# Kernel optimization log

Measured on AMD Instinct MI355X. Metric: run time of the kernel, lower is better.

Reference implementation:

```python
import jax, jax.numpy as jnp
import numpy as np

FEATURE_DIM = 16
NUM_HEADS = 16
HEAD_DIM = 64
R2 = float(np.sqrt(2.0))
RD = float(np.sqrt(FEATURE_DIM))        # sqrt(d) = 4
RRD = float(np.sqrt(RD))                # d^(1/4) = 2
RMS_EPS = 1e-5


def taylor_exp(x):
    # x: [b, h, l, d] -> [b, h, l, 1 + d + d*d]
    x2 = (x[..., :, None] * x[..., None, :]).reshape(*x.shape[:-1], FEATURE_DIM * FEATURE_DIM) / R2
    ones = jnp.ones_like(x[..., :1])
    return jnp.concatenate([ones, x / RRD, x2 / RD], axis=-1)


def setup_inputs() -> dict:
    key = jax.random.key(0)
    ks = jax.random.split(key, 5)
    b, l, d_model = 4, 2048, 1024
    inp = {
        'hidden_states': jax.random.normal(ks[0], (b, l, d_model), dtype=jnp.float32),
        'Wq': jax.random.normal(ks[1], (FEATURE_DIM * NUM_HEADS, d_model), dtype=jnp.float32) * 0.02,
        'Wk': jax.random.normal(ks[2], (FEATURE_DIM * NUM_HEADS, d_model), dtype=jnp.float32) * 0.02,
        'Wv': jax.random.normal(ks[3], (NUM_HEADS * HEAD_DIM, d_model), dtype=jnp.float32) * 0.02,
        'Wo': jax.random.normal(ks[4], (d_model, NUM_HEADS * HEAD_DIM), dtype=jnp.float32) * 0.02,
        'g_weight': jnp.ones((HEAD_DIM,), dtype=jnp.float32),
    }
    return inp


def reference(hidden_states, Wq, Wk, Wv, Wo, g_weight):
    b, l, _ = hidden_states.shape
    # projections (Linear, no bias): x @ W.T
    q = (hidden_states @ Wq.T).reshape(b, l, NUM_HEADS, FEATURE_DIM).transpose(0, 2, 1, 3)
    k = (hidden_states @ Wk.T).reshape(b, l, NUM_HEADS, FEATURE_DIM).transpose(0, 2, 1, 3)
    v = (hidden_states @ Wv.T).reshape(b, l, NUM_HEADS, HEAD_DIM).transpose(0, 2, 1, 3)

    qf = taylor_exp(q)  # [b, h, l, 273]
    kf = taylor_exp(k)  # [b, h, l, 273]

    A_qk = jnp.einsum('bhnd,bhmd->bhnm', qf, kf)
    A_qk = jnp.tril(A_qk)
    y = jnp.einsum('bhnm,bhme->bhne', A_qk, v)  # [b, h, l, head_dim]

    kv_state = jnp.einsum('bhnd,bhnf->bhfd', kf, v)[:, :, None]  # [b, h, 1, head_dim, 273]

    # RMSNorm over head_dim
    rms = jax.lax.rsqrt(jnp.mean(y * y, axis=-1, keepdims=True) + RMS_EPS)
    y = y * rms * g_weight

    y = y.transpose(0, 2, 1, 3).reshape(b, l, NUM_HEADS * HEAD_DIM)
    out = y @ Wo.T
    return out, kv_state
```

## Files before the change

kernel.cpp:

```cpp
#include <hip/hip_runtime.h>


typedef unsigned short u16;
typedef unsigned int u32;
typedef __attribute__((ext_vector_type(4))) float f32x4;
typedef __attribute__((ext_vector_type(16))) float f32x16;
typedef __attribute__((ext_vector_type(8))) short s16x8;

struct MaskT { static constexpr bool value = true;  };
struct MaskF { static constexpr bool value = false; };

__device__ __forceinline__ float bf2f(u16 u) {
    union { unsigned int i; float f; } x; x.i = ((unsigned int)u) << 16; return x.f;
}
__device__ __forceinline__ u16 f2bf(float f) {
    union { float f; unsigned int u; } x; x.f = f;
    unsigned int r = x.u + 0x7FFFu + ((x.u >> 16) & 1u);
    return (u16)(r >> 16);
}

typedef const __attribute__((address_space(1))) u32* gas1_t;
typedef __attribute__((address_space(3))) u32* las3_t;
__device__ __forceinline__ void gld16(const u16* g, u16* l) {
    __builtin_amdgcn_global_load_lds((gas1_t)(const void*)g, (las3_t)(void*)l, 16, 0, 0);
}

__global__ void detect_kernel(const unsigned int* __restrict__ H, int* __restrict__ flag)
{
    const int lane = threadIdx.x;
    int cnt = 0;
#pragma unroll
    for (int i = 0; i < 16; ++i) {
        const unsigned int wrd = H[lane * 16 + i];
        const int e = (int)((wrd >> 7) & 0xFFu);
        if (e >= 85 && e <= 170) ++cnt;
    }
    cnt += __shfl_xor(cnt, 1);  cnt += __shfl_xor(cnt, 2);
    cnt += __shfl_xor(cnt, 4);  cnt += __shfl_xor(cnt, 8);
    cnt += __shfl_xor(cnt, 16); cnt += __shfl_xor(cnt, 32);
    if (lane == 0) *flag = (cnt < 700) ? 1 : 0;
}

__global__ __launch_bounds__(256)
void cvt_all_kernel(const void* __restrict__ H,  const void* __restrict__ Wq,
                    const void* __restrict__ Wk, const void* __restrict__ Wv,
                    const void* __restrict__ Wo, const void* __restrict__ gw,
                    u16* __restrict__ Hb,  u16* __restrict__ Wqb,
                    u16* __restrict__ Wkb, u16* __restrict__ Wvb,
                    u16* __restrict__ Wob, u16* __restrict__ gwb,
                    const int* __restrict__ flag)
{
    const int f32in = *flag;
    const int NQ = 11010112 / 4;
    for (int qi = blockIdx.x * 256 + threadIdx.x; qi < NQ; qi += gridDim.x * 256) {
        const int i = qi * 4;
        const void* src; u16* dst; int off;
        if      (i <  8388608) { src = H;  dst = Hb;  off = i; }
        else if (i <  8650752) { src = Wq; dst = Wqb; off = i - 8388608; }
        else if (i <  8912896) { src = Wk; dst = Wkb; off = i - 8650752; }
        else if (i <  9961472) { src = Wv; dst = Wvb; off = i - 8912896; }
        else if (i < 11010048) { src = Wo; dst = Wob; off = i - 9961472; }
        else                   { src = gw; dst = gwb; off = i - 11010048; }
        ushort4 o;
        if (f32in) {
            const float4 v = *((const float4*)src + (off >> 2));
            o.x = f2bf(v.x); o.y = f2bf(v.y); o.z = f2bf(v.z); o.w = f2bf(v.w);
        } else {
            o = *((const ushort4*)src + (off >> 2));
        }
        *(ushort4*)(dst + off) = o;
    }
}

template<int MODE>
__global__ __launch_bounds__(256)
void gemm_nt(const u16* __restrict__ A,
             const u16* __restrict__ Bq, const u16* __restrict__ Bk,
             const u16* __restrict__ Bv,
             u16* __restrict__ Oq, u16* __restrict__ Ok,
             u16* __restrict__ Ovt, float* __restrict__ Of)
{
    __shared__ __attribute__((aligned(16))) u16 As[4096];
    __shared__ __attribute__((aligned(16))) u16 Bs[4096];
    const int t = threadIdx.x;
    const int lane = t & 63, w = t >> 6;
    const int c = lane & 15, qd = lane >> 4;
    const int wm = (w >> 1) * 64, wn = (w & 1) * 64;
    const int rm = blockIdx.y * 128;
    const int cb = blockIdx.x * 128;

    const u16* Bsrc; int wrow0;
    if (MODE == 0) {
        if (cb < 256)      { Bsrc = Bq; wrow0 = cb; }
        else if (cb < 512) { Bsrc = Bk; wrow0 = cb - 256; }
        else               { Bsrc = Bv; wrow0 = cb - 512; }
    } else { Bsrc = Bq; wrow0 = cb; }

    f32x4 acc[4][4];
#pragma unroll
    for (int i = 0; i < 4; ++i)
#pragma unroll
        for (int j = 0; j < 4; ++j) acc[i][j] = (f32x4){0.f, 0.f, 0.f, 0.f};

    const u16* Ag = A    + (size_t)(rm    + (t >> 2)) * 1024 + (t & 3) * 8;
    const u16* Bg = Bsrc + (size_t)(wrow0 + (t >> 2)) * 1024 + (t & 3) * 8;
    u16* AsW = As + w * 512;
    u16* BsW = Bs + w * 512;

    for (int kt = 0; kt < 32; ++kt) {
        const int k0 = kt * 32;
        __syncthreads();
        gld16(Ag + k0,         AsW);
        gld16(Ag + 65536 + k0, AsW + 2048);
        gld16(Bg + k0,         BsW);
        gld16(Bg + 65536 + k0, BsW + 2048);
        __syncthreads();
        s16x8 af[4], bfr[4];
#pragma unroll
        for (int mt = 0; mt < 4; ++mt) af[mt]  = *(const s16x8*)&As[(wm + mt * 16 + c) * 32 + qd * 8];
#pragma unroll
        for (int nt = 0; nt < 4; ++nt) bfr[nt] = *(const s16x8*)&Bs[(wn + nt * 16 + c) * 32 + qd * 8];
#pragma unroll
        for (int mt = 0; mt < 4; ++mt)
#pragma unroll
            for (int nt = 0; nt < 4; ++nt)
                acc[mt][nt] = __builtin_amdgcn_mfma_f32_16x16x32_bf16(af[mt], bfr[nt], acc[mt][nt], 0, 0, 0);
    }

#pragma unroll
    for (int mt = 0; mt < 4; ++mt) {
#pragma unroll
        for (int nt = 0; nt < 4; ++nt) {
            const int gc = cb + wn + nt * 16 + c;
            const int row0 = rm + wm + mt * 16 + qd * 4;
            if (MODE == 1) {
#pragma unroll
                for (int r = 0; r < 4; ++r)
                    Of[(size_t)(row0 + r) * 1024 + gc] = acc[mt][nt][r];
            } else if (gc < 512) {
#pragma unroll
                for (int r = 0; r < 4; ++r) {
                    const int row = row0 + r;
                    const int b_ = row >> 11, l_ = row & 2047;
                    const int cc = gc & 255;
                    const int h = cc >> 4, idx = cc & 15;
                    u16* dst = (gc < 256) ? Oq : Ok;
                    dst[(size_t)((b_ * 16 + h) * 2048 + l_) * 16 + idx] = f2bf(acc[mt][nt][r]);
                }
            } else {
                const int cc = gc - 512;
                const int h = cc >> 6, idx = cc & 63;
                const int b_ = row0 >> 11, l0 = row0 & 2047;
                ushort4 pk;
                pk.x = f2bf(acc[mt][nt][0]);
                pk.y = f2bf(acc[mt][nt][1]);
                pk.z = f2bf(acc[mt][nt][2]);
                pk.w = f2bf(acc[mt][nt][3]);
                *(ushort4*)(Ovt + ((size_t)((b_ * 16 + h) * 64 + idx)) * 2048 + l0) = pk;
            }
        }
    }
}

__global__ __launch_bounds__(512, 2)
void attn_kernel(const u16* __restrict__ Qg, const u16* __restrict__ Kg,
                 const u16* __restrict__ Vt, const u16* __restrict__ gwb,
                 u16* __restrict__ Yn)
{
    __shared__ __attribute__((aligned(16))) u16 Vs[2][8192];
    const int t = threadIdx.x, lane = t & 63, w = t >> 6;
    const int la = lane & 31, h = lane >> 5;
    const int pid = blockIdx.y * 4 + blockIdx.x;
    const int lid = (pid & 7) * 32 + (pid >> 3);
    const int bh = lid >> 2;
    const int jj = lid & 3;
    const int b_ = bh >> 4, hh = bh & 15;
    const u16* Qh = Qg + (size_t)bh * (2048 * 16);
    const u16* Kh = Kg + (size_t)bh * (2048 * 16);
    const u16* Vh = Vt + (size_t)bh * (64 * 2048);
    const float gl0 = bf2f(gwb[la]);
    const float gl1 = bf2f(gwb[32 + la]);
    const f32x16 z16 = {0.f,0.f,0.f,0.f,0.f,0.f,0.f,0.f,
                        0.f,0.f,0.f,0.f,0.f,0.f,0.f,0.f};
    const int vbase0 = (la << 8) | (h << 4);
    const int vsw = (la & 7) << 4;

    auto stageV = [&](int n0s, int bufsel) {
#pragma unroll
        for (int i = 0; i < 2; ++i) {
            const int slot = i * 512 + t;
            const int fl = slot >> 4;
            const int seg = (slot & 15) ^ (fl & 7);
            gld16(Vh + (size_t)fl * 2048 + n0s + seg * 8,
                  (u16*)Vs[bufsel] + (size_t)(i * 512 + (w << 6)) * 8);
        }
    };

    for (int pass = 0; pass < 2; ++pass) {
        const int qb = pass ? jj : (7 - jj);
        const int q0 = qb * 256 + w * 32;
        const int kf = 2 * qb + (w >> 2);
        const int wp = w & 3;
        const int nck = 2 * qb + 2;

        const s16x8 bq = *(const s16x8*)(Qh + (size_t)(q0 + la) * 16 + h * 8);
        f32x16 yt0 = z16, yt1 = z16;
        s16x8 ka[4];
        const char* vsc = (const char*)Vs[0];

        auto loadK = [&](s16x8* kk, int kcL) {
#pragma unroll
            for (int kt = 0; kt < 4; ++kt)
                kk[kt] = *(const s16x8*)(Kh + (size_t)(kcL * 128 + kt * 32 + la) * 16 + h * 8);
        };

        auto tile = [&](int kt, auto MASKED) {
            constexpr bool masked = decltype(MASKED)::value;
            f32x16 sv = __builtin_amdgcn_mfma_f32_32x32x16_bf16(ka[kt], bq, z16, 0, 0, 0);
            float p[16];
#pragma unroll
            for (int r = 0; r < 16; ++r) {
                const float s = sv[r];
                float pv = fmaf(s, fmaf(s, 0.03125f, 0.25f), 1.0f);
                if (masked) {
                    const int keyloc = (r & 3) + 8 * (r >> 2) + 4 * h;
                    if (keyloc > la) pv = 0.f;
                }
                p[r] = pv;
            }
#pragma unroll
            for (int ks = 0; ks < 2; ++ks) {
                u32 X0, X1, Y0, Y1;
                asm("v_cvt_pk_bf16_f32 %0, %1, %2" : "=v"(X0) : "v"(p[8*ks+0]), "v"(p[8*ks+1]));
                asm("v_cvt_pk_bf16_f32 %0, %1, %2" : "=v"(X1) : "v"(p[8*ks+2]), "v"(p[8*ks+3]));
                asm("v_cvt_pk_bf16_f32 %0, %1, %2" : "=v"(Y0) : "v"(p[8*ks+4]), "v"(p[8*ks+5]));
                asm("v_cvt_pk_bf16_f32 %0, %1, %2" : "=v"(Y1) : "v"(p[8*ks+6]), "v"(p[8*ks+7]));
                asm("v_permlane32_swap_b32 %0, %1" : "+v"(X0), "+v"(Y0));
                asm("v_permlane32_swap_b32 %0, %1" : "+v"(X1), "+v"(Y1));
                union { uint4 u; s16x8 v; } afu;
                afu.u = (uint4){X0, X1, Y0, Y1};
                const int offb = (kt << 6) | (ks << 5);
                const s16x8 vb0 = *(const s16x8*)(vsc + (((vbase0 + offb)) ^ vsw));
                const s16x8 vb1 = *(const s16x8*)(vsc + (((vbase0 + 8192 + offb)) ^ vsw));
                yt0 = __builtin_amdgcn_mfma_f32_32x32x16_bf16(afu.v, vb0, yt0, 0, 0, 0);
                yt1 = __builtin_amdgcn_mfma_f32_32x32x16_bf16(afu.v, vb1, yt1, 0, 0, 0);
            }
        };

        stageV(0, 0);
        loadK(ka, 0);
        __syncthreads();

        for (int kc = 0; kc < nck; ++kc) {
            const int cur = kc & 1;
            vsc = (const char*)Vs[cur];
            if (kc + 1 < nck) stageV((kc + 1) * 128, cur ^ 1);
            s16x8 kn[4] = {ka[0], ka[1], ka[2], ka[3]};
            if (kc < kf) loadK(kn, kc + 1);

            if (kc < kf) {
                tile(0, MaskF{}); tile(1, MaskF{});
                tile(2, MaskF{}); tile(3, MaskF{});
            } else if (kc == kf) {
                if (wp == 0)      { tile(0, MaskT{}); }
                else if (wp == 1) { tile(0, MaskF{}); tile(1, MaskT{}); }
                else if (wp == 2) { tile(0, MaskF{}); tile(1, MaskF{}); tile(2, MaskT{}); }
                else              { tile(0, MaskF{}); tile(1, MaskF{}); tile(2, MaskF{}); tile(3, MaskT{}); }
            }
            __syncthreads();
#pragma unroll
            for (int kt = 0; kt < 4; ++kt) ka[kt] = kn[kt];
        }

#pragma unroll
        for (int r = 0; r < 16; ++r) {
            float ss = yt0[r] * yt0[r] + yt1[r] * yt1[r];
            ss += __shfl_xor(ss, 1);  ss += __shfl_xor(ss, 2);
            ss += __shfl_xor(ss, 4);  ss += __shfl_xor(ss, 8);
            ss += __shfl_xor(ss, 16);
            const float rmsv = rsqrtf(ss * (1.0f / 64.0f) + 1e-5f);
            const int row = q0 + (r & 3) + 8 * (r >> 2) + 4 * h;
            u16* dst = Yn + ((size_t)(b_ * 2048 + row)) * 1024 + hh * 64;
            dst[la]      = f2bf(yt0[r] * rmsv * gl0);
            dst[32 + la] = f2bf(yt1[r] * rmsv * gl1);
        }
    }
}

__global__ __launch_bounds__(256)
void kv_mfma_kernel(const u16* __restrict__ Kg, const u16* __restrict__ Vt,
                    float* __restrict__ kvpart)
{
    __shared__ __attribute__((aligned(16))) float kS[64][20];
    __shared__ __attribute__((aligned(16))) float kT[64][20];
    __shared__ __attribute__((aligned(16))) u16 KFs[288][72];
    __shared__ __attribute__((aligned(16))) u16 Vs[64][72];
    const int t = threadIdx.x, lane = t & 63, w = t >> 6;
    const int c = lane & 15, qd = lane >> 4;
    const int ns = blockIdx.x, bh = blockIdx.y;
    const u16* Kh  = Kg + (size_t)bh * 2048 * 16;
    const u16* Vth = Vt + (size_t)bh * 64 * 2048;

    int i2a, j2a, i2b = 18, j2b = 18;
    {
        const int dd = t;
        if (dd == 0)      { i2a = 16; j2a = 17; }
        else if (dd < 17) { i2a = dd - 1; j2a = 16; }
        else              { i2a = (dd - 17) >> 4; j2a = (dd - 17) & 15; }
        if (t < 32) {
            const int d2 = 256 + t;
            if (d2 < 273) { i2b = (d2 - 17) >> 4; j2b = (d2 - 17) & 15; }
        }
    }

    f32x4 acc[4][5];
#pragma unroll
    for (int mt = 0; mt < 4; ++mt)
#pragma unroll
        for (int j = 0; j < 5; ++j) acc[mt][j] = (f32x4){0.f, 0.f, 0.f, 0.f};

    for (int ch = 0; ch < 8; ++ch) {
        const int n0 = ns * 512 + ch * 64;
        __syncthreads();
        if (t < 128) {
            const int row = t >> 1, half = t & 1;
            uint4 kv = *(const uint4*)(Kh + (size_t)(n0 + row) * 16 + half * 8);
            const u16* ke = (const u16*)&kv;
#pragma unroll
            for (int e = 0; e < 8; ++e) {
                const float f = bf2f(ke[e]);
                kS[row][half * 8 + e] = f;
                kT[row][half * 8 + e] = f * 0.17677669529663687f;
            }
        } else if (t < 192) {
            const int row = t - 128;
            kS[row][16] = 1.f;  kS[row][17] = 1.f;  kS[row][18] = 0.f;
            kT[row][16] = 0.5f; kT[row][17] = 1.f;  kT[row][18] = 0.f;
        }
#pragma unroll
        for (int i = 0; i < 2; ++i) {
            const int lin = i * 256 + t;
            const int f = lin >> 3, seg = lin & 7;
            *(uint4*)&Vs[f][seg * 8] =
                *(const uint4*)(Vth + (size_t)f * 2048 + n0 + seg * 8);
        }
        __syncthreads();
        {
            unsigned int* dst = (unsigned int*)&KFs[t][0];
#pragma unroll 8
            for (int i = 0; i < 32; ++i) {
                const float v0 = kS[2 * i][i2a]     * kT[2 * i][j2a];
                const float v1 = kS[2 * i + 1][i2a] * kT[2 * i + 1][j2a];
                dst[i] = (unsigned int)f2bf(v0) | ((unsigned int)f2bf(v1) << 16);
            }
            if (t < 32) {
                unsigned int* dst2 = (unsigned int*)&KFs[256 + t][0];
#pragma unroll 8
                for (int i = 0; i < 32; ++i) {
                    const float v0 = kS[2 * i][i2b]     * kT[2 * i][j2b];
                    const float v1 = kS[2 * i + 1][i2b] * kT[2 * i + 1][j2b];
                    dst2[i] = (unsigned int)f2bf(v0) | ((unsigned int)f2bf(v1) << 16);
                }
            }
        }
        __syncthreads();
#pragma unroll
        for (int kt = 0; kt < 2; ++kt) {
            s16x8 va[4];
#pragma unroll
            for (int mt = 0; mt < 4; ++mt)
                va[mt] = *(const s16x8*)&Vs[mt * 16 + c][kt * 32 + qd * 8];
#pragma unroll
            for (int j = 0; j < 5; ++j) {
                const int dt = w + 4 * j;
                if (dt < 18) {
                    s16x8 vb = *(const s16x8*)&KFs[dt * 16 + c][kt * 32 + qd * 8];
#pragma unroll
                    for (int mt = 0; mt < 4; ++mt)
                        acc[mt][j] = __builtin_amdgcn_mfma_f32_16x16x32_bf16(va[mt], vb, acc[mt][j], 0, 0, 0);
                }
            }
        }
    }

    float* base = kvpart + ((size_t)(ns * 64 + bh) * 64) * 273;
#pragma unroll
    for (int j = 0; j < 5; ++j) {
        const int dt = w + 4 * j;
        if (dt >= 18) continue;
        const int dd = dt * 16 + c;
        if (dd >= 273) continue;
#pragma unroll
        for (int mt = 0; mt < 4; ++mt)
#pragma unroll
            for (int r = 0; r < 4; ++r) {
                const int f = mt * 16 + qd * 4 + r;
                base[f * 273 + dd] = acc[mt][j][r];
            }
    }
}

__global__ __launch_bounds__(256)
void kv_fin_kernel(const float* __restrict__ kvpart, float* __restrict__ o)
{
    const int i = blockIdx.x * 256 + threadIdx.x;
    const int S = 64 * 64 * 273;
    if (i < S)
        o[i] = kvpart[i] + kvpart[i + S] + kvpart[i + 2 * S] + kvpart[i + 3 * S];
}

extern "C" void kernel_launch(void* const* d_in, const int* in_sizes, int n_in,
                              void* d_out, int out_size, void* d_ws, size_t ws_size,
                              hipStream_t stream)
{
    const void* H  = d_in[0];
    const void* Wq = d_in[1];
    const void* Wk = d_in[2];
    const void* Wv = d_in[3];
    const void* Wo = d_in[4];
    const void* gw = d_in[5];
    float* outf = (float*)d_out;

    char* ws = (char*)d_ws;
    const size_t M = 1 << 20;
    u16*   Hb    = (u16*)(ws);
    u16*   Wqb   = (u16*)(ws + 16 * M);
    u16*   Wkb   = (u16*)(ws + 16 * M + 512 * 1024);
    u16*   Wvb   = (u16*)(ws + 17 * M);
    u16*   Wob   = (u16*)(ws + 19 * M);
    u16*   gwb   = (u16*)(ws + 21 * M);
    int*   flag  = (int*)(ws + 21 * M + 4096);
    u16*   q     = (u16*)(ws + 22 * M);
    u16*   k     = (u16*)(ws + 26 * M);
    u16*   vt    = (u16*)(ws + 30 * M);
    float* kvpart= (float*)(ws + 46 * M);
    u16*   yn    = Hb;

    detect_kernel<<<1, 64, 0, stream>>>((const unsigned int*)H, flag);
    cvt_all_kernel<<<2048, 256, 0, stream>>>(H, Wq, Wk, Wv, Wo, gw,
                                             Hb, Wqb, Wkb, Wvb, Wob, gwb, flag);

    gemm_nt<0><<<dim3(12, 64), 256, 0, stream>>>(Hb, Wqb, Wkb, Wvb, q, k, vt, nullptr);
    attn_kernel<<<dim3(4, 64), 512, 0, stream>>>(q, k, vt, gwb, yn);
    kv_mfma_kernel<<<dim3(4, 64), 256, 0, stream>>>(k, vt, kvpart);
    kv_fin_kernel<<<4368, 256, 0, stream>>>(kvpart, outf + (size_t)8388608);
    gemm_nt<1><<<dim3(8, 64), 256, 0, stream>>>(yn, Wob, nullptr, nullptr,
                                                nullptr, nullptr, nullptr, outf);
}
```

Measured before the change: 240.7 us.

## Merge attention and kv-state kernels into one launch; widen GEMM K-tile with swizzle

Combines the causal attention kernel and the kv_state MFMA kernel into a single launch, partitioning blocks by index so that kv work runs concurrently with attention on otherwise idle CUs. This removes one launch and the serialization between the two kernels. The projection GEMM now loads 64-wide K tiles with XOR-swizzled LDS layout, halving loop iterations and barriers and avoiding bank conflicts, and remaps block IDs so neighbouring blocks land on the same XCD. The cost is more LDS per GEMM block, and kv blocks leave half of their threads idle under the 512-thread launch.

```diff
diff --git a/kernel.cpp b/kernel.cpp
--- a/kernel.cpp
+++ b/kernel.cpp
@@ -80,14 +80,17 @@
              u16* __restrict__ Oq, u16* __restrict__ Ok,
              u16* __restrict__ Ovt, float* __restrict__ Of)
 {
-    __shared__ __attribute__((aligned(16))) u16 As[4096];
-    __shared__ __attribute__((aligned(16))) u16 Bs[4096];
+    __shared__ __attribute__((aligned(16))) u16 As[8192];
+    __shared__ __attribute__((aligned(16))) u16 Bs[8192];
     const int t = threadIdx.x;
     const int lane = t & 63, w = t >> 6;
     const int c = lane & 15, qd = lane >> 4;
     const int wm = (w >> 1) * 64, wn = (w & 1) * 64;
-    const int rm = blockIdx.y * 128;
-    const int cb = blockIdx.x * 128;
+    const int nwgx = gridDim.x;
+    const int pid = blockIdx.y * nwgx + blockIdx.x;
+    const int lid = (pid & 7) * ((nwgx * 64) >> 3) + (pid >> 3);
+    const int rm = (lid / nwgx) * 128;
+    const int cb = (lid % nwgx) * 128;
 
     const u16* Bsrc; int wrow0;
     if (MODE == 0) {
@@ -102,29 +105,43 @@
 #pragma unroll
         for (int j = 0; j < 4; ++j) acc[i][j] = (f32x4){0.f, 0.f, 0.f, 0.f};
 
-    const u16* Ag = A    + (size_t)(rm    + (t >> 2)) * 1024 + (t & 3) * 8;
-    const u16* Bg = Bsrc + (size_t)(wrow0 + (t >> 2)) * 1024 + (t & 3) * 8;
+    const int r0 = w * 8 + (lane >> 3);
+    const int s0 = (lane & 7) ^ (lane >> 3);
+    const u16* Ag = A    + (size_t)(rm    + r0) * 1024 + s0 * 8;
+    const u16* Bg = Bsrc + (size_t)(wrow0 + r0) * 1024 + s0 * 8;
     u16* AsW = As + w * 512;
     u16* BsW = Bs + w * 512;
 
-    for (int kt = 0; kt < 32; ++kt) {
-        const int k0 = kt * 32;
+    for (int kt = 0; kt < 16; ++kt) {
+        const int k0 = kt * 64;
         __syncthreads();
-        gld16(Ag + k0,         AsW);
-        gld16(Ag + 65536 + k0, AsW + 2048);
-        gld16(Bg + k0,         BsW);
-        gld16(Bg + 65536 + k0, BsW + 2048);
+#pragma unroll
+        for (int i = 0; i < 4; ++i) {
+            gld16(Ag + (size_t)(i * 32) * 1024 + k0, AsW + i * 2048);
+            gld16(Bg + (size_t)(i * 32) * 1024 + k0, BsW + i * 2048);
+        }
         __syncthreads();
-        s16x8 af[4], bfr[4];
-#pragma unroll
-        for (int mt = 0; mt < 4; ++mt) af[mt]  = *(const s16x8*)&As[(wm + mt * 16 + c) * 32 + qd * 8];
-#pragma unroll
-        for (int nt = 0; nt < 4; ++nt) bfr[nt] = *(const s16x8*)&Bs[(wn + nt * 16 + c) * 32 + qd * 8];
-#pragma unroll
-        for (int mt = 0; mt < 4; ++mt)
-#pragma unroll
-            for (int nt = 0; nt < 4; ++nt)
-                acc[mt][nt] = __builtin_amdgcn_mfma_f32_16x16x32_bf16(af[mt], bfr[nt], acc[mt][nt], 0, 0, 0);
+        s16x8 af[2][4], bfr[2][4];
+#pragma unroll
+        for (int kk = 0; kk < 2; ++kk) {
+#pragma unroll
+            for (int mt = 0; mt < 4; ++mt) {
+                const int row = wm + mt * 16 + c;
+                af[kk][mt] = *(const s16x8*)&As[row * 64 + (((kk * 4 + qd) ^ (row & 7)) * 8)];
+            }
+#pragma unroll
+            for (int nt = 0; nt < 4; ++nt) {
+                const int row = wn + nt * 16 + c;
+                bfr[kk][nt] = *(const s16x8*)&Bs[row * 64 + (((kk * 4 + qd) ^ (row & 7)) * 8)];
+            }
+        }
+#pragma unroll
+        for (int kk = 0; kk < 2; ++kk)
+#pragma unroll
+            for (int mt = 0; mt < 4; ++mt)
+#pragma unroll
+                for (int nt = 0; nt < 4; ++nt)
+                    acc[mt][nt] = __builtin_amdgcn_mfma_f32_16x16x32_bf16(af[kk][mt], bfr[kk][nt], acc[mt][nt], 0, 0, 0);
     }
 
 #pragma unroll
@@ -162,241 +179,248 @@
     }
 }
 
-__global__ __launch_bounds__(512, 2)
-void attn_kernel(const u16* __restrict__ Qg, const u16* __restrict__ Kg,
-                 const u16* __restrict__ Vt, const u16* __restrict__ gwb,
-                 u16* __restrict__ Yn)
-{
-    __shared__ __attribute__((aligned(16))) u16 Vs[2][8192];
+__global__ __launch_bounds__(512, 4)
+void akv_kernel(const u16* __restrict__ Qg, const u16* __restrict__ Kg,
+                const u16* __restrict__ Vt, const u16* __restrict__ gwb,
+                u16* __restrict__ Yn, float* __restrict__ kvpart)
+{
+    __shared__ __attribute__((aligned(16))) char lds[61440];
     const int t = threadIdx.x, lane = t & 63, w = t >> 6;
-    const int la = lane & 31, h = lane >> 5;
-    const int pid = blockIdx.y * 4 + blockIdx.x;
-    const int lid = (pid & 7) * 32 + (pid >> 3);
-    const int bh = lid >> 2;
-    const int jj = lid & 3;
-    const int b_ = bh >> 4, hh = bh & 15;
-    const u16* Qh = Qg + (size_t)bh * (2048 * 16);
-    const u16* Kh = Kg + (size_t)bh * (2048 * 16);
-    const u16* Vh = Vt + (size_t)bh * (64 * 2048);
-    const float gl0 = bf2f(gwb[la]);
-    const float gl1 = bf2f(gwb[32 + la]);
-    const f32x16 z16 = {0.f,0.f,0.f,0.f,0.f,0.f,0.f,0.f,
-                        0.f,0.f,0.f,0.f,0.f,0.f,0.f,0.f};
-    const int vbase0 = (la << 8) | (h << 4);
-    const int vsw = (la & 7) << 4;
-
-    auto stageV = [&](int n0s, int bufsel) {
-#pragma unroll
-        for (int i = 0; i < 2; ++i) {
-            const int slot = i * 512 + t;
-            const int fl = slot >> 4;
-            const int seg = (slot & 15) ^ (fl & 7);
-            gld16(Vh + (size_t)fl * 2048 + n0s + seg * 8,
-                  (u16*)Vs[bufsel] + (size_t)(i * 512 + (w << 6)) * 8);
-        }
-    };
-
-    for (int pass = 0; pass < 2; ++pass) {
-        const int qb = pass ? jj : (7 - jj);
-        const int q0 = qb * 256 + w * 32;
-        const int kf = 2 * qb + (w >> 2);
-        const int wp = w & 3;
-        const int nck = 2 * qb + 2;
-
-        const s16x8 bq = *(const s16x8*)(Qh + (size_t)(q0 + la) * 16 + h * 8);
-        f32x16 yt0 = z16, yt1 = z16;
-        s16x8 ka[4];
-        const char* vsc = (const char*)Vs[0];
-
-        auto loadK = [&](s16x8* kk, int kcL) {
-#pragma unroll
-            for (int kt = 0; kt < 4; ++kt)
-                kk[kt] = *(const s16x8*)(Kh + (size_t)(kcL * 128 + kt * 32 + la) * 16 + h * 8);
+    const int pid = blockIdx.y * 8 + blockIdx.x;
+    const int x = pid & 7;
+    const int cc = pid >> 3;
+
+    if (cc < 32) {
+        const int la = lane & 31, h = lane >> 5;
+        const int bh = x * 8 + (cc >> 2);
+        const int jj = cc & 3;
+        const int b_ = bh >> 4, hh = bh & 15;
+        const u16* Qh = Qg + (size_t)bh * (2048 * 16);
+        const u16* Kh = Kg + (size_t)bh * (2048 * 16);
+        const u16* Vh = Vt + (size_t)bh * (64 * 2048);
+        const float gl0 = bf2f(gwb[la]);
+        const float gl1 = bf2f(gwb[32 + la]);
+        const f32x16 z16 = {0.f,0.f,0.f,0.f,0.f,0.f,0.f,0.f,
+                            0.f,0.f,0.f,0.f,0.f,0.f,0.f,0.f};
+        const int vbase0 = (la << 8) | (h << 4);
+        const int vsw = (la & 7) << 4;
+        u16* VsB = (u16*)lds;
+
+        auto stageV = [&](int n0s, int bufsel) {
+#pragma unroll
+            for (int i = 0; i < 2; ++i) {
+                const int slot = i * 512 + t;
+                const int fl = slot >> 4;
+                const int seg = (slot & 15) ^ (fl & 7);
+                gld16(Vh + (size_t)fl * 2048 + n0s + seg * 8,
+                      VsB + (size_t)bufsel * 8192 + (size_t)(i * 512 + (w << 6)) * 8);
+            }
         };
 
-        auto tile = [&](int kt, auto MASKED) {
-            constexpr bool masked = decltype(MASKED)::value;
-            f32x16 sv = __builtin_amdgcn_mfma_f32_32x32x16_bf16(ka[kt], bq, z16, 0, 0, 0);
-            float p[16];
+        for (int pass = 0; pass < 2; ++pass) {
+            const int qb = pass ? jj : (7 - jj);
+            const int q0 = qb * 256 + w * 32;
+            const int kf = 2 * qb + (w >> 2);
+            const int wp = w & 3;
+            const int nck = 2 * qb + 2;
+
+            const s16x8 bq = *(const s16x8*)(Qh + (size_t)(q0 + la) * 16 + h * 8);
+            f32x16 yt0 = z16, yt1 = z16;
+            s16x8 ka[4];
+            const char* vsc = (const char*)VsB;
+
+            auto loadK = [&](s16x8* kk, int kcL) {
+#pragma unroll
+                for (int kt = 0; kt < 4; ++kt)
+                    kk[kt] = *(const s16x8*)(Kh + (size_t)(kcL * 128 + kt * 32 + la) * 16 + h * 8);
+            };
+
+            auto tile = [&](int kt, auto MASKED) {
+                constexpr bool masked = decltype(MASKED)::value;
+                f32x16 sv = __builtin_amdgcn_mfma_f32_32x32x16_bf16(ka[kt], bq, z16, 0, 0, 0);
+                float p[16];
+#pragma unroll
+                for (int r = 0; r < 16; ++r) {
+                    const float s = sv[r];
+                    float pv = fmaf(s, fmaf(s, 0.03125f, 0.25f), 1.0f);
+                    if (masked) {
+                        const int keyloc = (r & 3) + 8 * (r >> 2) + 4 * h;
+                        if (keyloc > la) pv = 0.f;
+                    }
+                    p[r] = pv;
+                }
+#pragma unroll
+                for (int ks = 0; ks < 2; ++ks) {
+                    u32 X0, X1, Y0, Y1;
+                    asm("v_cvt_pk_bf16_f32 %0, %1, %2" : "=v"(X0) : "v"(p[8*ks+0]), "v"(p[8*ks+1]));
+                    asm("v_cvt_pk_bf16_f32 %0, %1, %2" : "=v"(X1) : "v"(p[8*ks+2]), "v"(p[8*ks+3]));
+                    asm("v_cvt_pk_bf16_f32 %0, %1, %2" : "=v"(Y0) : "v"(p[8*ks+4]), "v"(p[8*ks+5]));
+                    asm("v_cvt_pk_bf16_f32 %0, %1, %2" : "=v"(Y1) : "v"(p[8*ks+6]), "v"(p[8*ks+7]));
+                    asm("v_permlane32_swap_b32 %0, %1" : "+v"(X0), "+v"(Y0));
+                    asm("v_permlane32_swap_b32 %0, %1" : "+v"(X1), "+v"(Y1));
+                    union { uint4 u; s16x8 v; } afu;
+                    afu.u = (uint4){X0, X1, Y0, Y1};
+                    const int offb = (kt << 6) | (ks << 5);
+                    const s16x8 vb0 = *(const s16x8*)(vsc + (((vbase0 + offb)) ^ vsw));
+                    const s16x8 vb1 = *(const s16x8*)(vsc + (((vbase0 + 8192 + offb)) ^ vsw));
+                    yt0 = __builtin_amdgcn_mfma_f32_32x32x16_bf16(afu.v, vb0, yt0, 0, 0, 0);
+                    yt1 = __builtin_amdgcn_mfma_f32_32x32x16_bf16(afu.v, vb1, yt1, 0, 0, 0);
+                }
+            };
+
+            stageV(0, 0);
+            loadK(ka, 0);
+            __syncthreads();
+
+            for (int kc = 0; kc < nck; ++kc) {
+                const int cur = kc & 1;
+                vsc = (const char*)(VsB + (size_t)cur * 8192);
+                if (kc + 1 < nck) stageV((kc + 1) * 128, cur ^ 1);
+                s16x8 kn[4] = {ka[0], ka[1], ka[2], ka[3]};
+                if (kc < kf) loadK(kn, kc + 1);
+
+                if (kc < kf) {
+                    tile(0, MaskF{}); tile(1, MaskF{});
+                    tile(2, MaskF{}); tile(3, MaskF{});
+                } else if (kc == kf) {
+                    if (wp == 0)      { tile(0, MaskT{}); }
+                    else if (wp == 1) { tile(0, MaskF{}); tile(1, MaskT{}); }
+                    else if (wp == 2) { tile(0, MaskF{}); tile(1, MaskF{}); tile(2, MaskT{}); }
+                    else              { tile(0, MaskF{}); tile(1, MaskF{}); tile(2, MaskF{}); tile(3, MaskT{}); }
+                }
+                __syncthreads();
+#pragma unroll
+                for (int kt = 0; kt < 4; ++kt) ka[kt] = kn[kt];
+            }
+
 #pragma unroll
             for (int r = 0; r < 16; ++r) {
-                const float s = sv[r];
-                float pv = fmaf(s, fmaf(s, 0.03125f, 0.25f), 1.0f);
-                if (masked) {
-                    const int keyloc = (r & 3) + 8 * (r >> 2) + 4 * h;
-                    if (keyloc > la) pv = 0.f;
-                }
-                p[r] = pv;
-            }
-#pragma unroll
-            for (int ks = 0; ks < 2; ++ks) {
-                u32 X0, X1, Y0, Y1;
-                asm("v_cvt_pk_bf16_f32 %0, %1, %2" : "=v"(X0) : "v"(p[8*ks+0]), "v"(p[8*ks+1]));
-                asm("v_cvt_pk_bf16_f32 %0, %1, %2" : "=v"(X1) : "v"(p[8*ks+2]), "v"(p[8*ks+3]));
-                asm("v_cvt_pk_bf16_f32 %0, %1, %2" : "=v"(Y0) : "v"(p[8*ks+4]), "v"(p[8*ks+5]));
-                asm("v_cvt_pk_bf16_f32 %0, %1, %2" : "=v"(Y1) : "v"(p[8*ks+6]), "v"(p[8*ks+7]));
-                asm("v_permlane32_swap_b32 %0, %1" : "+v"(X0), "+v"(Y0));
-                asm("v_permlane32_swap_b32 %0, %1" : "+v"(X1), "+v"(Y1));
-                union { uint4 u; s16x8 v; } afu;
-                afu.u = (uint4){X0, X1, Y0, Y1};
-                const int offb = (kt << 6) | (ks << 5);
-                const s16x8 vb0 = *(const s16x8*)(vsc + (((vbase0 + offb)) ^ vsw));
-                const s16x8 vb1 = *(const s16x8*)(vsc + (((vbase0 + 8192 + offb)) ^ vsw));
-                yt0 = __builtin_amdgcn_mfma_f32_32x32x16_bf16(afu.v, vb0, yt0, 0, 0, 0);
-                yt1 = __builtin_amdgcn_mfma_f32_32x32x16_bf16(afu.v, vb1, yt1, 0, 0, 0);
-            }
-        };
-
-        stageV(0, 0);
-        loadK(ka, 0);
-        __syncthreads();
-
-        for (int kc = 0; kc < nck; ++kc) {
-            const int cur = kc & 1;
-            vsc = (const char*)Vs[cur];
-            if (kc + 1 < nck) stageV((kc + 1) * 128, cur ^ 1);
-            s16x8 kn[4] = {ka[0], ka[1], ka[2], ka[3]};
-            if (kc < kf) loadK(kn, kc + 1);
-
-            if (kc < kf) {
-                tile(0, MaskF{}); tile(1, MaskF{});
-                tile(2, MaskF{}); tile(3, MaskF{});
-            } else if (kc == kf) {
-                if (wp == 0)      { tile(0, MaskT{}); }
-                else if (wp == 1) { tile(0, MaskF{}); tile(1, MaskT{}); }
-                else if (wp == 2) { tile(0, MaskF{}); tile(1, MaskF{}); tile(2, MaskT{}); }
-                else              { tile(0, MaskF{}); tile(1, MaskF{}); tile(2, MaskF{}); tile(3, MaskT{}); }
-            }
+                float ss = yt0[r] * yt0[r] + yt1[r] * yt1[r];
+                ss += __shfl_xor(ss, 1);  ss += __shfl_xor(ss, 2);
+                ss += __shfl_xor(ss, 4);  ss += __shfl_xor(ss, 8);
+                ss += __shfl_xor(ss, 16);
+                const float rmsv = rsqrtf(ss * (1.0f / 64.0f) + 1e-5f);
+                const int row = q0 + (r & 3) + 8 * (r >> 2) + 4 * h;
+                u16* dst = Yn + ((size_t)(b_ * 2048 + row)) * 1024 + hh * 64;
+                dst[la]      = f2bf(yt0[r] * rmsv * gl0);
+                dst[32 + la] = f2bf(yt1[r] * rmsv * gl1);
+            }
+        }
+    } else {
+        const int c2 = cc - 32;
+        const int bh = x * 8 + (c2 >> 2);
+        const int ns = c2 & 3;
+        const int c = lane & 15, qd = lane >> 4;
+        const u16* Kh  = Kg + (size_t)bh * 2048 * 16;
+        const u16* Vth = Vt + (size_t)bh * 64 * 2048;
+        float (*kS)[20] = (float(*)[20])(lds);
+        float (*kT)[20] = (float(*)[20])(lds + 5120);
+        u16 (*KFs)[72]  = (u16(*)[72])(lds + 10240);
+        u16 (*Vs)[72]   = (u16(*)[72])(lds + 51712);
+
+        int i2a = 18, j2a = 18, i2b = 18, j2b = 18;
+        if (t < 256) {
+            const int dd = t;
+            if (dd == 0)      { i2a = 16; j2a = 17; }
+            else if (dd < 17) { i2a = dd - 1; j2a = 16; }
+            else              { i2a = (dd - 17) >> 4; j2a = (dd - 17) & 15; }
+            if (t < 32) {
+                const int d2 = 256 + t;
+                if (d2 < 273) { i2b = (d2 - 17) >> 4; j2b = (d2 - 17) & 15; }
+            }
+        }
+
+        f32x4 acc[4][5];
+#pragma unroll
+        for (int mt = 0; mt < 4; ++mt)
+#pragma unroll
+            for (int j = 0; j < 5; ++j) acc[mt][j] = (f32x4){0.f, 0.f, 0.f, 0.f};
+
+        for (int ch = 0; ch < 8; ++ch) {
+            const int n0 = ns * 512 + ch * 64;
             __syncthreads();
-#pragma unroll
-            for (int kt = 0; kt < 4; ++kt) ka[kt] = kn[kt];
-        }
-
-#pragma unroll
-        for (int r = 0; r < 16; ++r) {
-            float ss = yt0[r] * yt0[r] + yt1[r] * yt1[r];
-            ss += __shfl_xor(ss, 1);  ss += __shfl_xor(ss, 2);
-            ss += __shfl_xor(ss, 4);  ss += __shfl_xor(ss, 8);
-            ss += __shfl_xor(ss, 16);
-            const float rmsv = rsqrtf(ss * (1.0f / 64.0f) + 1e-5f);
-            const int row = q0 + (r & 3) + 8 * (r >> 2) + 4 * h;
-            u16* dst = Yn + ((size_t)(b_ * 2048 + row)) * 1024 + hh * 64;
-            dst[la]      = f2bf(yt0[r] * rmsv * gl0);
-            dst[32 + la] = f2bf(yt1[r] * rmsv * gl1);
-        }
-    }
-}
-
-__global__ __launch_bounds__(256)
-void kv_mfma_kernel(const u16* __restrict__ Kg, const u16* __restrict__ Vt,
-                    float* __restrict__ kvpart)
-{
-    __shared__ __attribute__((aligned(16))) float kS[64][20];
-    __shared__ __attribute__((aligned(16))) float kT[64][20];
-    __shared__ __attribute__((aligned(16))) u16 KFs[288][72];
-    __shared__ __attribute__((aligned(16))) u16 Vs[64][72];
-    const int t = threadIdx.x, lane = t & 63, w = t >> 6;
-    const int c = lane & 15, qd = lane >> 4;
-    const int ns = blockIdx.x, bh = blockIdx.y;
-    const u16* Kh  = Kg + (size_t)bh * 2048 * 16;
-    const u16* Vth = Vt + (size_t)bh * 64 * 2048;
-
-    int i2a, j2a, i2b = 18, j2b = 18;
-    {
-        const int dd = t;
-        if (dd == 0)      { i2a = 16; j2a = 17; }
-        else if (dd < 17) { i2a = dd - 1; j2a = 16; }
-        else              { i2a = (dd - 17) >> 4; j2a = (dd - 17) & 15; }
-        if (t < 32) {
-            const int d2 = 256 + t;
-            if (d2 < 273) { i2b = (d2 - 17) >> 4; j2b = (d2 - 17) & 15; }
-        }
-    }
-
-    f32x4 acc[4][5];
-#pragma unroll
-    for (int mt = 0; mt < 4; ++mt)
-#pragma unroll
-        for (int j = 0; j < 5; ++j) acc[mt][j] = (f32x4){0.f, 0.f, 0.f, 0.f};
-
-    for (int ch = 0; ch < 8; ++ch) {
-        const int n0 = ns * 512 + ch * 64;
-        __syncthreads();
-        if (t < 128) {
-            const int row = t >> 1, half = t & 1;
-            uint4 kv = *(const uint4*)(Kh + (size_t)(n0 + row) * 16 + half * 8);
-            const u16* ke = (const u16*)&kv;
-#pragma unroll
-            for (int e = 0; e < 8; ++e) {
-                const float f = bf2f(ke[e]);
-                kS[row][half * 8 + e] = f;
-                kT[row][half * 8 + e] = f * 0.17677669529663687f;
-            }
-        } else if (t < 192) {
-            const int row = t - 128;
-            kS[row][16] = 1.f;  kS[row][17] = 1.f;  kS[row][18] = 0.f;
-            kT[row][16] = 0.5f; kT[row][17] = 1.f;  kT[row][18] = 0.f;
-        }
-#pragma unroll
-        for (int i = 0; i < 2; ++i) {
-            const int lin = i * 256 + t;
-            const int f = lin >> 3, seg = lin & 7;
-            *(uint4*)&Vs[f][seg * 8] =
-                *(const uint4*)(Vth + (size_t)f * 2048 + n0 + seg * 8);
-        }
-        __syncthreads();
-        {
-            unsigned int* dst = (unsigned int*)&KFs[t][0];
-#pragma unroll 8
-            for (int i = 0; i < 32; ++i) {
-                const float v0 = kS[2 * i][i2a]     * kT[2 * i][j2a];
-                const float v1 = kS[2 * i + 1][i2a] * kT[2 * i + 1][j2a];
-                dst[i] = (unsigned int)f2bf(v0) | ((unsigned int)f2bf(v1) << 16);
-            }
-            if (t < 32) {
-                unsigned int* dst2 = (unsigned int*)&KFs[256 + t][0];
+            if (t < 128) {
+                const int row = t >> 1, half = t & 1;
+                uint4 kv = *(const uint4*)(Kh + (size_t)(n0 + row) * 16 + half * 8);
+                const u16* ke = (const u16*)&kv;
+#pragma unroll
+                for (int e = 0; e < 8; ++e) {
+                    const float f = bf2f(ke[e]);
+                    kS[row][half * 8 + e] = f;
+                    kT[row][half * 8 + e] = f * 0.17677669529663687f;
+                }
+            } else if (t < 192) {
+                const int row = t - 128;
+                kS[row][16] = 1.f;  kS[row][17] = 1.f;  kS[row][18] = 0.f;
+                kT[row][16] = 0.5f; kT[row][17] = 1.f;  kT[row][18] = 0.f;
+            }
+            if (t < 256) {
+#pragma unroll
+                for (int i = 0; i < 2; ++i) {
+                    const int lin = i * 256 + t;
+                    const int f = lin >> 3, seg = lin & 7;
+                    *(uint4*)&Vs[f][seg * 8] =
+                        *(const uint4*)(Vth + (size_t)f * 2048 + n0 + seg * 8);
+                }
+            }
+            __syncthreads();
+            if (t < 256) {
+                unsigned int* dst = (unsigned int*)&KFs[t][0];
 #pragma unroll 8
                 for (int i = 0; i < 32; ++i) {
-                    const float v0 = kS[2 * i][i2b]     * kT[2 * i][j2b];
-                    const float v1 = kS[2 * i + 1][i2b] * kT[2 * i + 1][j2b];
-                    dst2[i] = (unsigned int)f2bf(v0) | ((unsigned int)f2bf(v1) << 16);
-                }
-            }
-        }
-        __syncthreads();
-#pragma unroll
-        for (int kt = 0; kt < 2; ++kt) {
-            s16x8 va[4];
-#pragma unroll
-            for (int mt = 0; mt < 4; ++mt)
-                va[mt] = *(const s16x8*)&Vs[mt * 16 + c][kt * 32 + qd * 8];
+                    const float v0 = kS[2 * i][i2a]     * kT[2 * i][j2a];
+                    const float v1 = kS[2 * i + 1][i2a] * kT[2 * i + 1][j2a];
+                    dst[i] = (unsigned int)f2bf(v0) | ((unsigned int)f2bf(v1) << 16);
+                }
+                if (t < 32) {
+                    unsigned int* dst2 = (unsigned int*)&KFs[256 + t][0];
+#pragma unroll 8
+                    for (int i = 0; i < 32; ++i) {
+                        const float v0 = kS[2 * i][i2b]     * kT[2 * i][j2b];
+                        const float v1 = kS[2 * i + 1][i2b] * kT[2 * i + 1][j2b];
+                        dst2[i] = (unsigned int)f2bf(v0) | ((unsigned int)f2bf(v1) << 16);
+                    }
+                }
+            }
+            __syncthreads();
+            if (t < 256) {
+#pragma unroll
+                for (int kt = 0; kt < 2; ++kt) {
+                    s16x8 va[4];
+#pragma unroll
+                    for (int mt = 0; mt < 4; ++mt)
+                        va[mt] = *(const s16x8*)&Vs[mt * 16 + c][kt * 32 + qd * 8];
+#pragma unroll
+                    for (int j = 0; j < 5; ++j) {
+                        const int dt = w + 4 * j;
+                        if (dt < 18) {
+                            s16x8 vb = *(const s16x8*)&KFs[dt * 16 + c][kt * 32 + qd * 8];
+#pragma unroll
+                            for (int mt = 0; mt < 4; ++mt)
+                                acc[mt][j] = __builtin_amdgcn_mfma_f32_16x16x32_bf16(va[mt], vb, acc[mt][j], 0, 0, 0);
+                        }
+                    }
+                }
+            }
+        }
+
+        if (t < 256) {
+            float* base = kvpart + ((size_t)(ns * 64 + bh) * 64) * 273;
 #pragma unroll
             for (int j = 0; j < 5; ++j) {
                 const int dt = w + 4 * j;
-                if (dt < 18) {
-                    s16x8 vb = *(const s16x8*)&KFs[dt * 16 + c][kt * 32 + qd * 8];
-#pragma unroll
-                    for (int mt = 0; mt < 4; ++mt)
-                        acc[mt][j] = __builtin_amdgcn_mfma_f32_16x16x32_bf16(va[mt], vb, acc[mt][j], 0, 0, 0);
-                }
-            }
-        }
-    }
-
-    float* base = kvpart + ((size_t)(ns * 64 + bh) * 64) * 273;
-#pragma unroll
-    for (int j = 0; j < 5; ++j) {
-        const int dt = w + 4 * j;
-        if (dt >= 18) continue;
-        const int dd = dt * 16 + c;
-        if (dd >= 273) continue;
-#pragma unroll
-        for (int mt = 0; mt < 4; ++mt)
-#pragma unroll
-            for (int r = 0; r < 4; ++r) {
-                const int f = mt * 16 + qd * 4 + r;
-                base[f * 273 + dd] = acc[mt][j][r];
-            }
+                if (dt >= 18) continue;
+                const int dd = dt * 16 + c;
+                if (dd >= 273) continue;
+#pragma unroll
+                for (int mt = 0; mt < 4; ++mt)
+#pragma unroll
+                    for (int r = 0; r < 4; ++r) {
+                        const int f = mt * 16 + qd * 4 + r;
+                        base[f * 273 + dd] = acc[mt][j][r];
+                    }
+            }
+        }
     }
 }
 
@@ -441,8 +465,7 @@
                                              Hb, Wqb, Wkb, Wvb, Wob, gwb, flag);
 
     gemm_nt<0><<<dim3(12, 64), 256, 0, stream>>>(Hb, Wqb, Wkb, Wvb, q, k, vt, nullptr);
-    attn_kernel<<<dim3(4, 64), 512, 0, stream>>>(q, k, vt, gwb, yn);
-    kv_mfma_kernel<<<dim3(4, 64), 256, 0, stream>>>(k, vt, kvpart);
+    akv_kernel<<<dim3(8, 64), 512, 0, stream>>>(q, k, vt, gwb, yn, kvpart);
     kv_fin_kernel<<<4368, 256, 0, stream>>>(kvpart, outf + (size_t)8388608);
     gemm_nt<1><<<dim3(8, 64), 256, 0, stream>>>(yn, Wob, nullptr, nullptr,
                                                 nullptr, nullptr, nullptr, outf);
```

Result: faster. 228.0 us (-5.3%).
